# Optimization experiments

Hardware: AMD Instinct MI355X
Metric: run time of the kernel (lower is better)

The kernel has to match this reference:

```python
import jax, jax.numpy as jnp
import numpy as np


def setup_inputs() -> dict:
    key = jax.random.key(0)
    ks = jax.random.split(key, 8)
    E = 2_000_000          # num facts (edges)
    B, M = 8, 2000         # batch, max_local_entity -> B*M = 16000 entity slots
    R, D = 2000, 128       # num relations, hidden size (in_features == out_features)
    return {
        "local_entity": jax.random.randint(ks[0], (B, M), 0, M),
        "batch_heads": jax.random.randint(ks[1], (E,), 0, B * M),
        "batch_tails": jax.random.randint(ks[2], (E,), 0, B * M),
        "batch_rels": jax.random.randint(ks[3], (E,), 0, R),
        "val_one": jax.random.uniform(ks[4], (E,), dtype=jnp.float32),
        "rel_features": jax.random.normal(ks[5], (R, D), dtype=jnp.float32),
        "W": jax.random.normal(ks[6], (D, D), dtype=jnp.float32) * 0.05,
        "b": jax.random.normal(ks[7], (D,), dtype=jnp.float32) * 0.05,
    }


def reference(local_entity, batch_heads, batch_tails, batch_rels, val_one,
              rel_features, W, b):
    B, M = local_entity.shape
    num_ent = B * M
    # gather relation features per fact, linear transform (nn.Linear: x @ W.T + b)
    fact_rel = rel_features[batch_rels]            # [E, D]
    fact_val = fact_rel @ W.T + b                  # [E, D]
    # sparse COO mm == weighted scatter-add of fact_val into entity slots
    weighted = fact_val * val_one[:, None]         # [E, D]
    tail_agg = jax.ops.segment_sum(weighted, batch_tails, num_segments=num_ent)
    head_agg = jax.ops.segment_sum(weighted, batch_heads, num_segments=num_ent)
    f2e_emb = jax.nn.relu(tail_agg + head_agg)     # [B*M, D]
    return f2e_emb.reshape(B, M, -1)
```

## Files before the change

### kernel.cpp

```cpp
#include <hip/hip_runtime.h>
#include <hip/hip_bf16.h>
#include <cstdint>

typedef _Float16 half2v __attribute__((ext_vector_type(2)));

#define EPB   16
#define MAXNB 1024
#define FPB   4096
#define FPT   4
#define SORTCAP 4608
#define CPT   9
#define OVFCAP 65536


__global__ __launch_bounds__(1024) void bin_rwb_kernel(
    const int* __restrict__ heads, const int* __restrict__ tails,
    const int* __restrict__ rels, const float* __restrict__ val,
    const float* __restrict__ relf, const float* __restrict__ W,
    const float* __restrict__ bias, _Float16* __restrict__ rwb,
    int* __restrict__ gcnt, int* __restrict__ ovfcnt, uint2* __restrict__ ovf,
    unsigned* __restrict__ slots,
    int E, int R, int NB, int CAPB) {
    __shared__ int cnt[MAXNB];
    __shared__ int gbase[MAXNB];
    const int t = threadIdx.x;
    for (int k = t; k < NB; k += 1024) cnt[k] = 0;
    __syncthreads();

    const int i0 = blockIdx.x * FPB + t * FPT;
    unsigned payT[FPT], payH[FPT], prT[FPT], prH[FPT];
#pragma unroll
    for (int u = 0; u < FPT; ++u) { prT[u] = 0xFFFFFFFFu; prH[u] = 0xFFFFFFFFu; }

    int tl[FPT], hd[FPT], rr[FPT];
    float vv[FPT];
    int nval = 0;
    if (i0 + FPT <= E) {
        const int4 T  = *reinterpret_cast<const int4*>(tails + i0);
        const int4 H  = *reinterpret_cast<const int4*>(heads + i0);
        const int4 Rv = *reinterpret_cast<const int4*>(rels + i0);
        const float4 Vv = *reinterpret_cast<const float4*>(val + i0);
        tl[0] = T.x;  tl[1] = T.y;  tl[2] = T.z;  tl[3] = T.w;
        hd[0] = H.x;  hd[1] = H.y;  hd[2] = H.z;  hd[3] = H.w;
        rr[0] = Rv.x; rr[1] = Rv.y; rr[2] = Rv.z; rr[3] = Rv.w;
        vv[0] = Vv.x; vv[1] = Vv.y; vv[2] = Vv.z; vv[3] = Vv.w;
        nval = FPT;
    } else {
#pragma unroll
        for (int u = 0; u < FPT; ++u) {
            const int i = i0 + u;
            if (i < E) {
                tl[u] = tails[i]; hd[u] = heads[i];
                rr[u] = rels[i];  vv[u] = val[i];
                nval = u + 1;
            }
        }
    }
#pragma unroll
    for (int u = 0; u < FPT; ++u) {
        if (u < nval) {
            const unsigned hv =
                (unsigned)__builtin_bit_cast(unsigned short, (_Float16)vv[u]);
            const int bt = tl[u] >> 4, bh = hd[u] >> 4;
            payT[u] = ((unsigned)(tl[u] & 15) << 28) | ((unsigned)rr[u] << 16) | hv;
            payH[u] = ((unsigned)(hd[u] & 15) << 28) | ((unsigned)rr[u] << 16) | hv;
            const int rt = atomicAdd(&cnt[bt], 1);
            const int rh = atomicAdd(&cnt[bh], 1);
            prT[u] = ((unsigned)bt << 16) | (unsigned)rt;
            prH[u] = ((unsigned)bh << 16) | (unsigned)rh;
        }
    }
    __syncthreads();
    for (int k = t; k < NB; k += 1024) {
        const int c = cnt[k];
        gbase[k] = c ? atomicAdd(&gcnt[k], c) : 0;
    }
    __syncthreads();
#pragma unroll
    for (int u = 0; u < FPT; ++u) {
        if (prT[u] != 0xFFFFFFFFu) {
            {
                const int b1 = (int)(prT[u] >> 16);
                const int pos = gbase[b1] + (int)(prT[u] & 0xFFFFu);
                if (pos < CAPB) slots[(size_t)b1 * CAPB + pos] = payT[u];
                else {
                    const int op = atomicAdd(ovfcnt, 1);
                    if (op < OVFCAP) {
                        uint2 o;
                        o.x = ((unsigned)b1 << 16) | ((payT[u] >> 28) << 12) |
                              ((payT[u] >> 16) & 0xFFFu);
                        o.y = __float_as_uint(vv[u]);
                        ovf[op] = o;
                    }
                }
            }
            {
                const int b1 = (int)(prH[u] >> 16);
                const int pos = gbase[b1] + (int)(prH[u] & 0xFFFFu);
                if (pos < CAPB) slots[(size_t)b1 * CAPB + pos] = payH[u];
                else {
                    const int op = atomicAdd(ovfcnt, 1);
                    if (op < OVFCAP) {
                        uint2 o;
                        o.x = ((unsigned)b1 << 16) | ((payH[u] >> 28) << 12) |
                              ((payH[u] >> 16) & 0xFFFu);
                        o.y = __float_as_uint(vv[u]);
                        ovf[op] = o;
                    }
                }
            }
        }
    }

    const int rsub = t >> 7;
    const int col  = t & 127;
    for (int row0 = blockIdx.x * 8; row0 < R; row0 += gridDim.x * 8) {
        const int row = row0 + rsub;
        if (row < R) {
            const float4* rp = reinterpret_cast<const float4*>(relf + (size_t)row * 128);
            const float4* wp = reinterpret_cast<const float4*>(W + (size_t)col * 128);
            float acc = 0.f;
#pragma unroll
            for (int i = 0; i < 32; ++i) {
                float4 a = rp[i], w = wp[i];
                acc += a.x * w.x + a.y * w.y + a.z * w.z + a.w * w.w;
            }
            rwb[(size_t)row * 128 + col] = (_Float16)(acc + bias[col]);
        }
    }
}

#define GATHER_BATCH8(S0, J, A0, A1)                                            \
    {                                                                           \
        uint2 qp[4];                                                            \
        _Pragma("unroll")                                                       \
        for (int u = 0; u < 4; ++u)                                             \
            qp[u] = *reinterpret_cast<const uint2*>(&se[(S0) + (J) + 2 * u]);   \
        unsigned qs[8];                                                         \
        _Pragma("unroll")                                                       \
        for (int u = 0; u < 4; ++u) {                                           \
            qs[2 * u]     = __builtin_amdgcn_readfirstlane(qp[u].x);            \
            qs[2 * u + 1] = __builtin_amdgcn_readfirstlane(qp[u].y);            \
        }                                                                       \
        unsigned rw[8];                                                         \
        _Pragma("unroll")                                                       \
        for (int u = 0; u < 8; ++u) {                                           \
            const _Float16* rowp = rwb + (size_t)((qs[u] >> 16) & 0xFFFu) * 128;\
            rw[u] = *reinterpret_cast<const unsigned*>(rowp + loff);            \
        }                                                                       \
        _Pragma("unroll")                                                       \
        for (int u = 0; u < 8; ++u) {                                           \
            asm("v_fma_mix_f32 %[d], %[s0], %[s1], %[d] op_sel:[0,0,0] op_sel_hi:[1,1,0]" \
                : [d]"+v"(A0) : [s0]"s"(qs[u]), [s1]"v"(rw[u]));                \
            asm("v_fma_mix_f32 %[d], %[s0], %[s1], %[d] op_sel:[0,1,0] op_sel_hi:[1,1,0]" \
                : [d]"+v"(A1) : [s0]"s"(qs[u]), [s1]"v"(rw[u]));                \
        }                                                                       \
    }

#define GATHER_BATCH8x2(S0A, JA, A0A, A1A, S0B, JB, A0B, A1B)                   \
    {                                                                           \
        uint2 qpa[4], qpb[4];                                                   \
        _Pragma("unroll")                                                       \
        for (int u = 0; u < 4; ++u) {                                           \
            qpa[u] = *reinterpret_cast<const uint2*>(&se[(S0A) + (JA) + 2 * u]);\
            qpb[u] = *reinterpret_cast<const uint2*>(&se[(S0B) + (JB) + 2 * u]);\
        }                                                                       \
        unsigned qsa[8], qsb[8];                                                \
        _Pragma("unroll")                                                       \
        for (int u = 0; u < 4; ++u) {                                           \
            qsa[2 * u]     = __builtin_amdgcn_readfirstlane(qpa[u].x);          \
            qsa[2 * u + 1] = __builtin_amdgcn_readfirstlane(qpa[u].y);          \
            qsb[2 * u]     = __builtin_amdgcn_readfirstlane(qpb[u].x);          \
            qsb[2 * u + 1] = __builtin_amdgcn_readfirstlane(qpb[u].y);          \
        }                                                                       \
        unsigned rwa[8], rwb_[8];                                               \
        _Pragma("unroll")                                                       \
        for (int u = 0; u < 8; ++u) {                                           \
            rwa[u] = *reinterpret_cast<const unsigned*>(                        \
                rwb + (size_t)((qsa[u] >> 16) & 0xFFFu) * 128 + loff);          \
            rwb_[u] = *reinterpret_cast<const unsigned*>(                       \
                rwb + (size_t)((qsb[u] >> 16) & 0xFFFu) * 128 + loff);          \
        }                                                                       \
        _Pragma("unroll")                                                       \
        for (int u = 0; u < 8; ++u) {                                           \
            asm("v_fma_mix_f32 %[d], %[s0], %[s1], %[d] op_sel:[0,0,0] op_sel_hi:[1,1,0]" \
                : [d]"+v"(A0A) : [s0]"s"(qsa[u]), [s1]"v"(rwa[u]));             \
            asm("v_fma_mix_f32 %[d], %[s0], %[s1], %[d] op_sel:[0,1,0] op_sel_hi:[1,1,0]" \
                : [d]"+v"(A1A) : [s0]"s"(qsa[u]), [s1]"v"(rwa[u]));             \
            asm("v_fma_mix_f32 %[d], %[s0], %[s1], %[d] op_sel:[0,0,0] op_sel_hi:[1,1,0]" \
                : [d]"+v"(A0B) : [s0]"s"(qsb[u]), [s1]"v"(rwb_[u]));            \
            asm("v_fma_mix_f32 %[d], %[s0], %[s1], %[d] op_sel:[0,1,0] op_sel_hi:[1,1,0]" \
                : [d]"+v"(A1B) : [s0]"s"(qsb[u]), [s1]"v"(rwb_[u]));            \
        }                                                                       \
    }

__global__ __launch_bounds__(512) void gather_kernel(
    const unsigned* __restrict__ slots, const int* __restrict__ gcnt,
    const int* __restrict__ ovfcnt, const uint2* __restrict__ ovf,
    const _Float16* __restrict__ rwb, float* __restrict__ out,
    int NUMENT, int CAPB) {
    __shared__ unsigned se[SORTCAP];
    __shared__ int cnt[EPB], basep[EPB];
    const int t = threadIdx.x;
    const int b = blockIdx.x;
    if (t < EPB) cnt[t] = 0;
    __syncthreads();

    int deg = gcnt[b];
    if (deg > CAPB) deg = CAPB;
    const unsigned* sl = slots + (size_t)b * CAPB;

    unsigned e[CPT];
    int rk[CPT];
#pragma unroll
    for (int u = 0; u < CPT; ++u) {
        const int k = t + u * 512;
        rk[u] = -1;
        if (k < deg) {
            e[u] = sl[k];
            rk[u] = atomicAdd(&cnt[(int)(e[u] >> 28)], 1);
        }
    }
    __syncthreads();
    if (t == 0) {
        int s = 0;
#pragma unroll
        for (int i = 0; i < EPB; ++i) { basep[i] = s; s += cnt[i]; }
    }
    __syncthreads();
#pragma unroll
    for (int u = 0; u < CPT; ++u)
        if (rk[u] >= 0) se[basep[(int)(e[u] >> 28)] + rk[u]] = e[u];
    __syncthreads();

    const int novf = min(*ovfcnt, OVFCAP);

    const int wv = t >> 6, lane = t & 63;
    const int loff = lane * 2;

    const int leA = wv * 2, leB = leA + 1;
    const int s0A = basep[leA], cA = cnt[leA];
    const int s0B = basep[leB], cB = cnt[leB];
    float a0A = 0.f, a1A = 0.f, a0B = 0.f, a1B = 0.f;
    int jA = 0, jB = 0;
    while (jA + 8 <= cA && jB + 8 <= cB) {
        GATHER_BATCH8x2(s0A, jA, a0A, a1A, s0B, jB, a0B, a1B);
        jA += 8; jB += 8;
    }
    for (; jA + 8 <= cA; jA += 8) GATHER_BATCH8(s0A, jA, a0A, a1A);
    for (; jB + 8 <= cB; jB += 8) GATHER_BATCH8(s0B, jB, a0B, a1B);
    for (; jA < cA; ++jA) {
        const unsigned q = se[s0A + jA];
        const unsigned qs = __builtin_amdgcn_readfirstlane(q);
        const unsigned rwv = *reinterpret_cast<const unsigned*>(
            rwb + (size_t)((qs >> 16) & 0xFFFu) * 128 + loff);
        asm("v_fma_mix_f32 %[d], %[s0], %[s1], %[d] op_sel:[0,0,0] op_sel_hi:[1,1,0]"
            : [d]"+v"(a0A) : [s0]"s"(qs), [s1]"v"(rwv));
        asm("v_fma_mix_f32 %[d], %[s0], %[s1], %[d] op_sel:[0,1,0] op_sel_hi:[1,1,0]"
            : [d]"+v"(a1A) : [s0]"s"(qs), [s1]"v"(rwv));
    }
    for (; jB < cB; ++jB) {
        const unsigned q = se[s0B + jB];
        const unsigned qs = __builtin_amdgcn_readfirstlane(q);
        const unsigned rwv = *reinterpret_cast<const unsigned*>(
            rwb + (size_t)((qs >> 16) & 0xFFFu) * 128 + loff);
        asm("v_fma_mix_f32 %[d], %[s0], %[s1], %[d] op_sel:[0,0,0] op_sel_hi:[1,1,0]"
            : [d]"+v"(a0B) : [s0]"s"(qs), [s1]"v"(rwv));
        asm("v_fma_mix_f32 %[d], %[s0], %[s1], %[d] op_sel:[0,1,0] op_sel_hi:[1,1,0]"
            : [d]"+v"(a1B) : [s0]"s"(qs), [s1]"v"(rwv));
    }
    for (int k = 0; k < novf; ++k) {
        const uint2 o = ovf[k];
        if ((int)(o.x >> 16) == b) {
            const int ole = (int)((o.x >> 12) & 15u);
            if (ole == leA || ole == leB) {
                const int orel = (int)(o.x & 0xFFFu);
                const float ov = __uint_as_float(o.y);
                const unsigned orw = *reinterpret_cast<const unsigned*>(
                    rwb + (size_t)orel * 128 + loff);
                const half2v oh = __builtin_bit_cast(half2v, orw);
                if (ole == leA) { a0A += ov * (float)oh[0]; a1A += ov * (float)oh[1]; }
                else            { a0B += ov * (float)oh[0]; a1B += ov * (float)oh[1]; }
            }
        }
    }
    {
        const int ventA = b * EPB + leA;
        if (ventA < NUMENT) {
            float* op = out + (size_t)ventA * 128 + loff;
            float2 o2; o2.x = fmaxf(a0A, 0.f); o2.y = fmaxf(a1A, 0.f);
            *reinterpret_cast<float2*>(op) = o2;
        }
        const int ventB = b * EPB + leB;
        if (ventB < NUMENT) {
            float* op = out + (size_t)ventB * 128 + loff;
            float2 o2; o2.x = fmaxf(a0B, 0.f); o2.y = fmaxf(a1B, 0.f);
            *reinterpret_cast<float2*>(op) = o2;
        }
    }
}

__global__ void rwb_f32_kernel(const float* __restrict__ rel, const float* __restrict__ W,
                               const float* __restrict__ b, float* __restrict__ rwb, int R) {
    const int k = blockIdx.x;
    const int n = threadIdx.x;
    __shared__ float relk[128];
    relk[n] = rel[(size_t)k * 128 + n];
    __syncthreads();
    const float4* w4 = reinterpret_cast<const float4*>(W + (size_t)n * 128);
    const float4* r4 = reinterpret_cast<const float4*>(relk);
    float acc = 0.f;
#pragma unroll
    for (int i = 0; i < 32; ++i) {
        float4 a = r4[i], w = w4[i];
        acc += a.x * w.x + a.y * w.y + a.z * w.z + a.w * w.w;
    }
    rwb[(size_t)k * 128 + n] = acc + b[n];
}

__global__ void scatter_vec_kernel(const int* __restrict__ heads, const int* __restrict__ tails,
                                   const int* __restrict__ rels, const float* __restrict__ val,
                                   const float* __restrict__ rwb, float* __restrict__ out,
                                   long long nitems) {
    const long long i = (long long)blockIdx.x * blockDim.x + threadIdx.x;
    if (i >= nitems) return;
    const int e = (int)(i >> 5);
    const int c = (int)(i & 31) * 4;
    const float v = val[e];
    float4 rw = *reinterpret_cast<const float4*>(rwb + (size_t)rels[e] * 128 + c);
    float* pt = out + (size_t)tails[e] * 128 + c;
    float* ph = out + (size_t)heads[e] * 128 + c;
    unsafeAtomicAdd(pt + 0, v * rw.x); unsafeAtomicAdd(pt + 1, v * rw.y);
    unsafeAtomicAdd(pt + 2, v * rw.z); unsafeAtomicAdd(pt + 3, v * rw.w);
    unsafeAtomicAdd(ph + 0, v * rw.x); unsafeAtomicAdd(ph + 1, v * rw.y);
    unsafeAtomicAdd(ph + 2, v * rw.z); unsafeAtomicAdd(ph + 3, v * rw.w);
}

__global__ void relu_kernel(float* __restrict__ out, int n4) {
    const int i = blockIdx.x * blockDim.x + threadIdx.x;
    if (i >= n4) return;
    float4* p = reinterpret_cast<float4*>(out) + i;
    float4 v = *p;
    v.x = fmaxf(v.x, 0.f); v.y = fmaxf(v.y, 0.f);
    v.z = fmaxf(v.z, 0.f); v.w = fmaxf(v.w, 0.f);
    *p = v;
}

extern "C" void kernel_launch(void* const* d_in, const int* in_sizes, int n_in,
                              void* d_out, int out_size, void* d_ws, size_t ws_size,
                              hipStream_t stream) {
    const int* heads = (const int*)d_in[1];
    const int* tails = (const int*)d_in[2];
    const int* rels  = (const int*)d_in[3];
    const float* val  = (const float*)d_in[4];
    const float* relf = (const float*)d_in[5];
    const float* W    = (const float*)d_in[6];
    const float* b    = (const float*)d_in[7];
    float* out = (float*)d_out;

    const int NUMENT = in_sizes[0];
    const int E      = in_sizes[1];
    const int D      = in_sizes[7];
    const int R      = in_sizes[5] / D;

    const int NB = (NUMENT + EPB - 1) / EPB;
    const long long mean = (2LL * E * EPB) / (NUMENT > 0 ? NUMENT : 1);
    int CAPB = (int)(mean + mean / 16 + 256);

    const size_t rwb_bytes = (size_t)R * D * sizeof(_Float16);
    const size_t off_ctrl  = (rwb_bytes + 255) & ~(size_t)255;
    const size_t ctrl_b    = (size_t)(NB + 1) * sizeof(int);
    const size_t off_ovf   = (off_ctrl + ctrl_b + 255) & ~(size_t)255;
    const size_t ovf_b     = (size_t)OVFCAP * sizeof(uint2);
    const size_t off_slots = (off_ovf + ovf_b + 255) & ~(size_t)255;
    const size_t slots_b   = (size_t)NB * CAPB * sizeof(unsigned);

    if (NB <= MAXNB && R < 4096 && CAPB <= SORTCAP &&
        ws_size >= off_slots + slots_b) {
        _Float16* rwb   = (_Float16*)d_ws;
        int* gcnt       = (int*)((char*)d_ws + off_ctrl);
        int* ovfcnt     = gcnt + NB;
        uint2* ovf      = (uint2*)((char*)d_ws + off_ovf);
        unsigned* slots = (unsigned*)((char*)d_ws + off_slots);

        hipMemsetAsync(gcnt, 0, ctrl_b, stream);
        bin_rwb_kernel<<<(E + FPB - 1) / FPB, 1024, 0, stream>>>(
            heads, tails, rels, val, relf, W, b, rwb,
            gcnt, ovfcnt, ovf, slots, E, R, NB, CAPB);
        gather_kernel<<<NB, 512, 0, stream>>>(
            slots, gcnt, ovfcnt, ovf, rwb, out, NUMENT, CAPB);
    } else {
        float* rwb = (float*)d_ws;
        hipMemsetAsync(out, 0, (size_t)out_size * sizeof(float), stream);
        rwb_f32_kernel<<<R, 128, 0, stream>>>(relf, W, b, rwb, R);
        const long long items = (long long)E * 32;
        scatter_vec_kernel<<<(unsigned)((items + 255) / 256), 256, 0, stream>>>(
            heads, tails, rels, val, rwb, out, items);
        relu_kernel<<<(out_size / 4 + 255) / 256, 256, 0, stream>>>(out, out_size / 4);
    }
}
```

Measured before the change: 185.8 us.

## Pad per-block bin reservations to 16-slot granules and double facts per block

Each binning block now reserves bin slots in multiples of 16 and fills the unused padding with a marker value, so scattered slot writes land in aligned chunks. The gather kernel skips marked entries. Facts per block and facts per thread are doubled, with the bin capacity, sort capacity and per-thread gather count raised to match. The aim is to cut global atomics and partial-line writes. The cost is padding that wastes slot memory and gather bandwidth, plus larger per-thread register arrays.

```diff
diff --git a/kernel.cpp b/kernel.cpp
--- a/kernel.cpp
+++ b/kernel.cpp
@@ -6,10 +6,12 @@
 
 #define EPB   16
 #define MAXNB 1024
-#define FPB   4096
-#define FPT   4
-#define SORTCAP 4608
-#define CPT   9
+#define FPB   8192
+#define FPT   8
+#define GRAN  16
+#define MARK  0xFFFFFFFFu
+#define SORTCAP 7168
+#define CPT   14
 #define OVFCAP 65536
 
 
@@ -36,14 +38,14 @@
     float vv[FPT];
     int nval = 0;
     if (i0 + FPT <= E) {
-        const int4 T  = *reinterpret_cast<const int4*>(tails + i0);
-        const int4 H  = *reinterpret_cast<const int4*>(heads + i0);
-        const int4 Rv = *reinterpret_cast<const int4*>(rels + i0);
-        const float4 Vv = *reinterpret_cast<const float4*>(val + i0);
-        tl[0] = T.x;  tl[1] = T.y;  tl[2] = T.z;  tl[3] = T.w;
-        hd[0] = H.x;  hd[1] = H.y;  hd[2] = H.z;  hd[3] = H.w;
-        rr[0] = Rv.x; rr[1] = Rv.y; rr[2] = Rv.z; rr[3] = Rv.w;
-        vv[0] = Vv.x; vv[1] = Vv.y; vv[2] = Vv.z; vv[3] = Vv.w;
+        *reinterpret_cast<int4*>(&tl[0]) = *reinterpret_cast<const int4*>(tails + i0);
+        *reinterpret_cast<int4*>(&tl[4]) = *reinterpret_cast<const int4*>(tails + i0 + 4);
+        *reinterpret_cast<int4*>(&hd[0]) = *reinterpret_cast<const int4*>(heads + i0);
+        *reinterpret_cast<int4*>(&hd[4]) = *reinterpret_cast<const int4*>(heads + i0 + 4);
+        *reinterpret_cast<int4*>(&rr[0]) = *reinterpret_cast<const int4*>(rels + i0);
+        *reinterpret_cast<int4*>(&rr[4]) = *reinterpret_cast<const int4*>(rels + i0 + 4);
+        *reinterpret_cast<float4*>(&vv[0]) = *reinterpret_cast<const float4*>(val + i0);
+        *reinterpret_cast<float4*>(&vv[4]) = *reinterpret_cast<const float4*>(val + i0 + 4);
         nval = FPT;
     } else {
 #pragma unroll
@@ -73,7 +75,8 @@
     __syncthreads();
     for (int k = t; k < NB; k += 1024) {
         const int c = cnt[k];
-        gbase[k] = c ? atomicAdd(&gcnt[k], c) : 0;
+        const int rc = (c + GRAN - 1) & ~(GRAN - 1);
+        gbase[k] = rc ? atomicAdd(&gcnt[k], rc) : 0;
     }
     __syncthreads();
 #pragma unroll
@@ -111,6 +114,15 @@
             }
         }
     }
+    for (int k = t; k < NB; k += 1024) {
+        const int c = cnt[k];
+        const int rc = (c + GRAN - 1) & ~(GRAN - 1);
+        const int gb = gbase[k];
+        for (int p = c; p < rc; ++p) {
+            const int pos = gb + p;
+            if (pos < CAPB) slots[(size_t)k * CAPB + pos] = MARK;
+        }
+    }
 
     const int rsub = t >> 7;
     const int col  = t & 127;
@@ -218,7 +230,8 @@
         rk[u] = -1;
         if (k < deg) {
             e[u] = sl[k];
-            rk[u] = atomicAdd(&cnt[(int)(e[u] >> 28)], 1);
+            if (e[u] != MARK)
+                rk[u] = atomicAdd(&cnt[(int)(e[u] >> 28)], 1);
         }
     }
     __syncthreads();
@@ -364,8 +377,10 @@
     const int R      = in_sizes[5] / D;
 
     const int NB = (NUMENT + EPB - 1) / EPB;
+    const int NBLK = (E + FPB - 1) / FPB;
     const long long mean = (2LL * E * EPB) / (NUMENT > 0 ? NUMENT : 1);
-    int CAPB = (int)(mean + mean / 16 + 256);
+    int CAPB = (int)(mean + (long long)NBLK * 9 + mean / 16 + 256);
+    CAPB = (CAPB + GRAN - 1) & ~(GRAN - 1);
 
     const size_t rwb_bytes = (size_t)R * D * sizeof(_Float16);
     const size_t off_ctrl  = (rwb_bytes + 255) & ~(size_t)255;
@@ -384,7 +399,7 @@
         unsigned* slots = (unsigned*)((char*)d_ws + off_slots);
 
         hipMemsetAsync(gcnt, 0, ctrl_b, stream);
-        bin_rwb_kernel<<<(E + FPB - 1) / FPB, 1024, 0, stream>>>(
+        bin_rwb_kernel<<<NBLK, 1024, 0, stream>>>(
             heads, tails, rels, val, relf, W, b, rwb,
             gcnt, ovfcnt, ovf, slots, E, R, NB, CAPB);
         gather_kernel<<<NB, 512, 0, stream>>>(
```

After: 205.6 us. +10.7%, slower.

## Stage binned facts in shared memory and write bins out contiguously per block

Applied to the files above, without the earlier changes.

The binning kernel now sorts each block's fact payloads into a shared-memory buffer by bucket, using a block-wide prefix scan over bucket counts. It then writes each bucket's run to global slots with consecutive lanes, replacing scattered per-fact stores with coalesced ones. The block size drops to 512 threads with 8 facts per thread, and the rwb row stride changes to match. This adds a 32KB shared buffer and extra syncs, which may reduce occupancy, and overflow values are now rebuilt from fp16 rather than the original fp32.

```diff
diff --git a/kernel.cpp b/kernel.cpp
--- a/kernel.cpp
+++ b/kernel.cpp
@@ -7,13 +7,13 @@
 #define EPB   16
 #define MAXNB 1024
 #define FPB   4096
-#define FPT   4
+#define FPT   8
 #define SORTCAP 4608
 #define CPT   9
 #define OVFCAP 65536
 
 
-__global__ __launch_bounds__(1024) void bin_rwb_kernel(
+__global__ __launch_bounds__(512) void bin_rwb_kernel(
     const int* __restrict__ heads, const int* __restrict__ tails,
     const int* __restrict__ rels, const float* __restrict__ val,
     const float* __restrict__ relf, const float* __restrict__ W,
@@ -23,8 +23,11 @@
     int E, int R, int NB, int CAPB) {
     __shared__ int cnt[MAXNB];
     __shared__ int gbase[MAXNB];
+    __shared__ int lbase[MAXNB];
+    __shared__ int wsum[8];
+    __shared__ unsigned sse[2 * FPB];
     const int t = threadIdx.x;
-    for (int k = t; k < NB; k += 1024) cnt[k] = 0;
+    for (int k = t; k < NB; k += 512) cnt[k] = 0;
     __syncthreads();
 
     const int i0 = blockIdx.x * FPB + t * FPT;
@@ -36,14 +39,14 @@
     float vv[FPT];
     int nval = 0;
     if (i0 + FPT <= E) {
-        const int4 T  = *reinterpret_cast<const int4*>(tails + i0);
-        const int4 H  = *reinterpret_cast<const int4*>(heads + i0);
-        const int4 Rv = *reinterpret_cast<const int4*>(rels + i0);
-        const float4 Vv = *reinterpret_cast<const float4*>(val + i0);
-        tl[0] = T.x;  tl[1] = T.y;  tl[2] = T.z;  tl[3] = T.w;
-        hd[0] = H.x;  hd[1] = H.y;  hd[2] = H.z;  hd[3] = H.w;
-        rr[0] = Rv.x; rr[1] = Rv.y; rr[2] = Rv.z; rr[3] = Rv.w;
-        vv[0] = Vv.x; vv[1] = Vv.y; vv[2] = Vv.z; vv[3] = Vv.w;
+        *reinterpret_cast<int4*>(&tl[0]) = *reinterpret_cast<const int4*>(tails + i0);
+        *reinterpret_cast<int4*>(&tl[4]) = *reinterpret_cast<const int4*>(tails + i0 + 4);
+        *reinterpret_cast<int4*>(&hd[0]) = *reinterpret_cast<const int4*>(heads + i0);
+        *reinterpret_cast<int4*>(&hd[4]) = *reinterpret_cast<const int4*>(heads + i0 + 4);
+        *reinterpret_cast<int4*>(&rr[0]) = *reinterpret_cast<const int4*>(rels + i0);
+        *reinterpret_cast<int4*>(&rr[4]) = *reinterpret_cast<const int4*>(rels + i0 + 4);
+        *reinterpret_cast<float4*>(&vv[0]) = *reinterpret_cast<const float4*>(val + i0);
+        *reinterpret_cast<float4*>(&vv[4]) = *reinterpret_cast<const float4*>(val + i0 + 4);
         nval = FPT;
     } else {
 #pragma unroll
@@ -71,50 +74,74 @@
         }
     }
     __syncthreads();
-    for (int k = t; k < NB; k += 1024) {
+
+    {
+        int c0 = (2 * t < NB) ? cnt[2 * t] : 0;
+        int c1 = (2 * t + 1 < NB) ? cnt[2 * t + 1] : 0;
+        const int pair = c0 + c1;
+        int x = pair;
+#pragma unroll
+        for (int d = 1; d < 64; d <<= 1) {
+            const int y = __shfl_up(x, d);
+            if ((t & 63) >= d) x += y;
+        }
+        if ((t & 63) == 63) wsum[t >> 6] = x;
+        __syncthreads();
+        if (t < 64) {
+            int v = (t < 8) ? wsum[t] : 0;
+#pragma unroll
+            for (int d = 1; d < 8; d <<= 1) {
+                const int y = __shfl_up(v, d);
+                if (t >= d) v += y;
+            }
+            if (t < 8) wsum[t] = v;
+        }
+        __syncthreads();
+        const int woff = (t >= 64) ? wsum[(t >> 6) - 1] : 0;
+        const int excl = x + woff - pair;
+        if (2 * t < NB)     lbase[2 * t] = excl;
+        if (2 * t + 1 < NB) lbase[2 * t + 1] = excl + c0;
+    }
+    for (int k = t; k < NB; k += 512) {
         const int c = cnt[k];
         gbase[k] = c ? atomicAdd(&gcnt[k], c) : 0;
     }
     __syncthreads();
+
 #pragma unroll
     for (int u = 0; u < FPT; ++u) {
         if (prT[u] != 0xFFFFFFFFu) {
-            {
-                const int b1 = (int)(prT[u] >> 16);
-                const int pos = gbase[b1] + (int)(prT[u] & 0xFFFFu);
-                if (pos < CAPB) slots[(size_t)b1 * CAPB + pos] = payT[u];
-                else {
-                    const int op = atomicAdd(ovfcnt, 1);
-                    if (op < OVFCAP) {
-                        uint2 o;
-                        o.x = ((unsigned)b1 << 16) | ((payT[u] >> 28) << 12) |
-                              ((payT[u] >> 16) & 0xFFFu);
-                        o.y = __float_as_uint(vv[u]);
-                        ovf[op] = o;
-                    }
+            sse[lbase[(int)(prT[u] >> 16)] + (int)(prT[u] & 0xFFFFu)] = payT[u];
+            sse[lbase[(int)(prH[u] >> 16)] + (int)(prH[u] & 0xFFFFu)] = payH[u];
+        }
+    }
+    __syncthreads();
+
+    const int wv = t >> 6, lane = t & 63;
+    for (int k = wv; k < NB; k += 8) {
+        const int len = cnt[k];
+        const int lb  = lbase[k];
+        const int gb  = gbase[k];
+        for (int off = lane; off < len; off += 64) {
+            const unsigned p = sse[lb + off];
+            const int pos = gb + off;
+            if (pos < CAPB) slots[(size_t)k * CAPB + pos] = p;
+            else {
+                const int op = atomicAdd(ovfcnt, 1);
+                if (op < OVFCAP) {
+                    uint2 o;
+                    o.x = ((unsigned)k << 16) | ((p >> 28) << 12) | ((p >> 16) & 0xFFFu);
+                    o.y = __float_as_uint(
+                        (float)__builtin_bit_cast(_Float16, (unsigned short)(p & 0xFFFFu)));
+                    ovf[op] = o;
                 }
             }
-            {
-                const int b1 = (int)(prH[u] >> 16);
-                const int pos = gbase[b1] + (int)(prH[u] & 0xFFFFu);
-                if (pos < CAPB) slots[(size_t)b1 * CAPB + pos] = payH[u];
-                else {
-                    const int op = atomicAdd(ovfcnt, 1);
-                    if (op < OVFCAP) {
-                        uint2 o;
-                        o.x = ((unsigned)b1 << 16) | ((payH[u] >> 28) << 12) |
-                              ((payH[u] >> 16) & 0xFFFu);
-                        o.y = __float_as_uint(vv[u]);
-                        ovf[op] = o;
-                    }
-                }
-            }
         }
     }
 
     const int rsub = t >> 7;
     const int col  = t & 127;
-    for (int row0 = blockIdx.x * 8; row0 < R; row0 += gridDim.x * 8) {
+    for (int row0 = blockIdx.x * 4; row0 < R; row0 += gridDim.x * 4) {
         const int row = row0 + rsub;
         if (row < R) {
             const float4* rp = reinterpret_cast<const float4*>(relf + (size_t)row * 128);
@@ -384,7 +411,7 @@
         unsigned* slots = (unsigned*)((char*)d_ws + off_slots);
 
         hipMemsetAsync(gcnt, 0, ctrl_b, stream);
-        bin_rwb_kernel<<<(E + FPB - 1) / FPB, 1024, 0, stream>>>(
+        bin_rwb_kernel<<<(E + FPB - 1) / FPB, 512, 0, stream>>>(
             heads, tails, rels, val, relf, W, b, rwb,
             gcnt, ovfcnt, ovf, slots, E, R, NB, CAPB);
         gather_kernel<<<NB, 512, 0, stream>>>(
```

Result: slower. 199.8 us (+7.5%).
